# Kernel optimization log

Measured on AMD Instinct MI355X. Metric: run time of the kernel, lower is better.

Reference implementation:

```python
import jax, jax.numpy as jnp
from jax import lax
import numpy as np

UNTIL_T = 25  # until_time in source
EPS = 1e-6
K_SEG = 5     # number of temporal groups produced by Segment()


def conv1d(x, w, b=None, padding=((0, 0),)):
    y = lax.conv_general_dilated(x, w, (1,), padding,
                                 dimension_numbers=('NCH', 'OIH', 'NCH'))
    return y if b is None else y + b[None, :, None]


def maxpool1d(x, k, s):
    return lax.reduce_window(x, -jnp.inf, lax.max, (1, 1, k), (1, 1, s), 'VALID')


def batchnorm(x, g, b):
    m = x.mean((0, 2), keepdims=True)
    v = x.var((0, 2), keepdims=True)
    return g[None, :, None] * (x - m) / jnp.sqrt(v + 1e-5) + b[None, :, None]


def miu(x, sign, a, b):
    # fuzzy membership predicate: sigmoid(sign * a_c * (x - b_c))
    return jax.nn.sigmoid(sign * a[None, :, None] * (x - b[None, :, None]))


def upsample2(x):
    B, C, L = x.shape
    return jax.image.resize(x, (B, C, 2 * L), method='linear')


def logic_and(x, w, padding=((0, 0),)):
    # weighted geometric-mean fuzzy AND: exp(conv(log x, softmax(w)))
    wn = jax.nn.softmax(w.reshape(w.shape[0], -1), -1).reshape(w.shape)
    return jax.nn.relu(jnp.exp(conv1d(jnp.log(jnp.clip(x, 0.0, 1.0) + EPS), wn, padding=padding)))


def logic_or(x, w, padding=((0, 0),)):
    # dual fuzzy OR: 1 - exp(conv(log(1-x), softmax(w)))
    wn = jax.nn.softmax(w.reshape(w.shape[0], -1), -1).reshape(w.shape)
    return jax.nn.relu(1.0 - jnp.exp(conv1d(jnp.log(1.0 - jnp.clip(x, 0.0, 1.0) + EPS), wn, padding=padding)))


def until(x, T):
    # Until(x)[t] = max_{1<=d<=T} min( min_{0<=s<d} x[t+s], x[t+d] ), zero right-pad
    L = x.shape[-1]
    xp = jnp.pad(x, ((0, 0), (0, 0), (0, T)))
    runmin = x
    out = jnp.zeros_like(x)  # x >= 0 so 0 is a valid lower bound
    for d in range(1, T + 1):  # small fixed unroll over until_time
        xs = xp[..., d:d + L]
        out = jnp.maximum(out, jnp.minimum(runmin, xs))
        runmin = jnp.minimum(runmin, xs)
    return out[..., :L - 1]  # crop to match kernel-2 logic convs


def forward(x, wave_w, bn_g, bn_b, miu_ap, miu_bp, miu_an, miu_bn,
            ae_w1, ae_b1, ae_w2, ae_b2, ae_w3, ae_b3, ae_w4, ae_b4,
            and2_w, or2_w, and_w, or_w,
            fc1_w, fc1_b, fc2_w, fc2_b, fc3_w, fc3_b):
    B = x.shape[0]
    # Basic predicate network: wavelet conv (k=32) + BN + ReLU + pool -> [B,16,343]
    xf = maxpool1d(jax.nn.relu(batchnorm(conv1d(x, wave_w), bn_g, bn_b)), 3, 2)
    x_pos = maxpool1d(miu(xf, 1.0, miu_ap, miu_bp), 3, 2)    # [B,16,171]
    x_neg = maxpool1d(miu(xf, -1.0, miu_an, miu_bn), 3, 2)   # [B,16,171]
    x_miu = jnp.concatenate([x_pos, x_neg], 1)               # [B,32,171]
    # AutoEncoder -> w, same shape as x_miu
    h = maxpool1d(jnp.tanh(conv1d(x_miu, ae_w1, ae_b1, ((1, 1),))), 3, 2)   # [B,64,85]
    h = maxpool1d(jax.nn.relu(conv1d(h, ae_w2, ae_b2, ((1, 1),))), 3, 2)    # [B,32,42]
    h = jnp.tanh(conv1d(upsample2(h), ae_w3, ae_b3, ((2, 2),)))             # [B,64,86]
    h = jax.nn.sigmoid(conv1d(upsample2(h), ae_w4, ae_b4, ((2, 2),)))       # [B,32,174]
    w = maxpool1d(h, 4, 1)                                                  # [B,32,171]
    # Temporal grouping: K_SEG activation-level bands over w (vectorized, no cat loop)
    lo = (jnp.arange(K_SEG, dtype=w.dtype) / K_SEG)[:, None, None, None]
    hi = (jnp.arange(1, K_SEG + 1, dtype=w.dtype) / K_SEG).at[-1].set(2.0)[:, None, None, None]
    masks = (w[None] >= lo) & (w[None] < hi)                 # [K,B,32,171]
    seg = jnp.where(masks, w[None], 0.0) * x_miu[None]       # select_w * x_miu per segment
    inp = jnp.transpose(seg, (1, 0, 2, 3)).reshape(B, K_SEG * 32, -1)  # [B,160,171]
    x_until = until(inp, UNTIL_T)                            # [B,160,170]
    x_and1 = logic_and(inp, and2_w)                          # [B,20,170]
    x_or1 = logic_or(inp, or2_w)                             # [B,20,170]
    x1 = jnp.concatenate([x_and1, x_or1, x_until], 1)        # [B,200,170]
    x_and2 = logic_and(x1, and_w, ((1, 0),))                 # causal same-pad -> [B,6,170]
    x_or2 = logic_or(x1, or_w, ((1, 0),))                    # [B,6,170]
    x2 = jnp.concatenate([x_and2, x_or2], 1)                 # [B,12,170]
    # Classifier (dropout = identity at inference), Linear over last dim (=170)
    h = jax.nn.relu(jnp.einsum('bcl,ol->bco', x2, fc1_w) + fc1_b)
    h = jax.nn.relu(jnp.einsum('bco,po->bcp', h, fc2_w) + fc2_b)
    return jnp.einsum('bcp,qp->bcq', h, fc3_w) + fc3_b       # [B,12,10]


def setup_inputs() -> dict:
    key = jax.random.key(0)
    ks = jax.random.split(key, 24)
    n = lambda k, shp, s: jax.random.normal(k, shp, jnp.float32) * s
    B = 128
    d = {
        'x': n(ks[0], (B, 1, 719), 1.0),
        'wave_w': n(ks[1], (16, 1, 32), 1.0 / np.sqrt(32)),
        'bn_g': jnp.ones((16,), jnp.float32),
        'bn_b': jnp.zeros((16,), jnp.float32),
        'miu_ap': 1.0 + n(ks[2], (16,), 0.1),
        'miu_bp': n(ks[3], (16,), 0.1),
        'miu_an': 1.0 + n(ks[4], (16,), 0.1),
        'miu_bn': n(ks[5], (16,), 0.1),
        'ae_w1': n(ks[6], (64, 32, 3), 1.0 / np.sqrt(96)),
        'ae_b1': jnp.zeros((64,), jnp.float32),
        'ae_w2': n(ks[7], (32, 64, 3), 1.0 / np.sqrt(192)),
        'ae_b2': jnp.zeros((32,), jnp.float32),
        'ae_w3': n(ks[8], (64, 32, 3), 1.0 / np.sqrt(96)),
        'ae_b3': jnp.zeros((64,), jnp.float32),
        'ae_w4': n(ks[9], (32, 64, 3), 1.0 / np.sqrt(192)),
        'ae_b4': jnp.zeros((32,), jnp.float32),
        'and2_w': n(ks[10], (20, 160, 2), 1.0),
        'or2_w': n(ks[11], (20, 160, 2), 1.0),
        'and_w': n(ks[12], (6, 200, 2), 1.0),
        'or_w': n(ks[13], (6, 200, 2), 1.0),
        'fc1_w': n(ks[14], (1024, 170), 1.0 / np.sqrt(170)),
        'fc1_b': jnp.zeros((1024,), jnp.float32),
        'fc2_w': n(ks[15], (256, 1024), 1.0 / np.sqrt(1024)),
        'fc2_b': jnp.zeros((256,), jnp.float32),
        'fc3_w': n(ks[16], (10, 256), 1.0 / np.sqrt(256)),
        'fc3_b': jnp.zeros((10,), jnp.float32),
    }
    return d


def reference(x, wave_w, bn_g, bn_b, miu_ap, miu_bp, miu_an, miu_bn,
              ae_w1, ae_b1, ae_w2, ae_b2, ae_w3, ae_b3, ae_w4, ae_b4,
              and2_w, or2_w, and_w, or_w,
              fc1_w, fc1_b, fc2_w, fc2_b, fc3_w, fc3_b):
    return forward(x, wave_w, bn_g, bn_b, miu_ap, miu_bp, miu_an, miu_bn,
                   ae_w1, ae_b1, ae_w2, ae_b2, ae_w3, ae_b3, ae_w4, ae_b4,
                   and2_w, or2_w, and_w, or_w,
                   fc1_w, fc1_b, fc2_w, fc2_b, fc3_w, fc3_b)
```

## Files before the change

kernel.cpp:

```cpp
#include <hip/hip_runtime.h>

#define TPB 256
static inline int cdiv(int a, int b){ return (a + b - 1) / b; }

#define EPSL 1e-6f
#define ACT_TANH 0
#define ACT_RELU 1
#define ACT_SIG  2
#define ACT_NONE 3

__device__ __forceinline__ float sigf(float x){ return 1.0f / (1.0f + __expf(-x)); }
__device__ __forceinline__ float clip01(float x){ return fminf(fmaxf(x, 0.f), 1.f); }

#define OFF_Y1   0
#define OFF_XF   1409024
#define OFF_XMIU 2111488
#define OFF_H1   2811904
#define OFF_INP  4384768
#define OFF_X1   7886848
#define OFF_TAIL 12238848
#define OFF_P1   0
#define OFF_P2   0
#define OFF_GP   0
#define OFF_X2P  OFF_INP
#define OFF_W1P  (OFF_INP + 294912 + 393216)
#define OFF_FC1H OFF_X1
#define OFF_STATS OFF_TAIL
#define OFF_BNP  (OFF_TAIL + 64)
#define OFF_WN   (OFF_TAIL + 64 + 512)

__global__ void k_softmax(const float* __restrict__ a2, const float* __restrict__ o2,
                          const float* __restrict__ aw, const float* __restrict__ ow,
                          float* __restrict__ wn){
  int blk = blockIdx.x;
  const float* src; float* dst; int n;
  if (blk < 20)      { src = a2 + blk*320;      dst = wn + blk*320;              n = 320; }
  else if (blk < 40) { src = o2 + (blk-20)*320; dst = wn + 6400 + (blk-20)*320;  n = 320; }
  else if (blk < 46) { src = aw + (blk-40)*400; dst = wn + 12800 + (blk-40)*400; n = 400; }
  else               { src = ow + (blk-46)*400; dst = wn + 15200 + (blk-46)*400; n = 400; }
  __shared__ float sh[TPB];
  float m = -1e30f;
  for (int i = threadIdx.x; i < n; i += TPB) m = fmaxf(m, src[i]);
  sh[threadIdx.x] = m; __syncthreads();
  for (int off = TPB/2; off > 0; off >>= 1){
    if (threadIdx.x < off) sh[threadIdx.x] = fmaxf(sh[threadIdx.x], sh[threadIdx.x+off]);
    __syncthreads();
  }
  m = sh[0]; __syncthreads();
  float s = 0.f;
  for (int i = threadIdx.x; i < n; i += TPB) s += expf(src[i] - m);
  sh[threadIdx.x] = s; __syncthreads();
  for (int off = TPB/2; off > 0; off >>= 1){
    if (threadIdx.x < off) sh[threadIdx.x] += sh[threadIdx.x+off];
    __syncthreads();
  }
  float inv = 1.0f / sh[0];
  __syncthreads();
  for (int i = threadIdx.x; i < n; i += TPB) dst[i] = expf(src[i] - m) * inv;
}

__global__ void k_conv_wave(const float* __restrict__ x, const float* __restrict__ ww,
                            float* __restrict__ y){
  int idx = blockIdx.x*blockDim.x + threadIdx.x;
  if (idx >= 128*16*688) return;
  int l = idx % 688; int t = idx / 688; int o = t & 15; int b = t >> 4;
  const float* xr = x + b*719 + l;
  const float* wr = ww + o*32;
  float s = 0.f;
  #pragma unroll
  for (int k = 0; k < 32; k++) s = fmaf(xr[k], wr[k], s);
  y[idx] = s;
}

__global__ void k_bn_part(const float* __restrict__ y, double* __restrict__ bnp){
  int c = blockIdx.x & 15, ch = blockIdx.x >> 4;
  double s = 0.0, s2 = 0.0;
  for (int i = threadIdx.x; i < 16*688; i += TPB){
    int b = ch*16 + i/688, l = i % 688;
    float v = y[(b*16 + c)*688 + l];
    s += (double)v; s2 += (double)v * (double)v;
  }
  __shared__ double sh[TPB], sh2[TPB];
  sh[threadIdx.x] = s; sh2[threadIdx.x] = s2; __syncthreads();
  for (int off = TPB/2; off > 0; off >>= 1){
    if (threadIdx.x < off){ sh[threadIdx.x] += sh[threadIdx.x+off]; sh2[threadIdx.x] += sh2[threadIdx.x+off]; }
    __syncthreads();
  }
  if (threadIdx.x == 0){ bnp[blockIdx.x] = sh[0]; bnp[128 + blockIdx.x] = sh2[0]; }
}

__global__ void k_bn_fin(const double* __restrict__ bnp, float* __restrict__ stats){
  int c = threadIdx.x;
  if (c >= 16) return;
  double s = 0.0, s2 = 0.0;
  for (int j = 0; j < 8; j++){ s += bnp[j*16 + c]; s2 += bnp[128 + j*16 + c]; }
  double n = 128.0*688.0;
  double m = s / n;
  double var = s2 / n - m*m;
  stats[c]      = (float)m;
  stats[16 + c] = (float)(1.0 / sqrt(var + 1e-5));
}

__global__ void k_xmiu2(const float* __restrict__ y, const float* __restrict__ stats,
                        const float* __restrict__ g, const float* __restrict__ bb,
                        const float* __restrict__ ap, const float* __restrict__ bp,
                        const float* __restrict__ an, const float* __restrict__ bn,
                        float* __restrict__ out){
  int idx = blockIdx.x*blockDim.x + threadIdx.x;
  if (idx >= 128*32*171) return;
  int l = idx % 171; int t = idx / 171; int c = t & 31; int b = t >> 5;
  int cc = c & 15;
  float mean = stats[cc], rstd = stats[16 + cc];
  float gc = g[cc], bc = bb[cc];
  float sign = (c < 16) ? 1.f : -1.f;
  float a  = (c < 16) ? ap[cc] : an[cc];
  float bo = (c < 16) ? bp[cc] : bn[cc];
  const float* yr = y + (b*16 + cc)*688 + 4*l;
  float v[7];
  #pragma unroll
  for (int i = 0; i < 7; i++)
    v[i] = fmaxf(fmaf(gc*(yr[i] - mean), rstd, bc), 0.f);
  float m = -1e30f;
  #pragma unroll
  for (int j = 0; j < 3; j++){
    float xf = fmaxf(fmaxf(v[2*j], v[2*j+1]), v[2*j+2]);
    m = fmaxf(m, sigf(sign * a * (xf - bo)));
  }
  out[idx] = m;
}

template<int SMODE, int LSRC, int LEFF>
__device__ __forceinline__ float stage_val(const float* __restrict__ src, int q){
  if (q < 0 || q >= LEFF) return 0.f;
  if constexpr (SMODE == 0){
    return src[q];
  } else if constexpr (SMODE == 1){
    float m = fmaxf(fmaxf(src[2*q], src[2*q+1]), src[2*q+2]);
    return tanhf(m);
  } else if constexpr (SMODE == 2){
    auto P = [&](int k){
      float m = fmaxf(fmaxf(src[2*k], src[2*k+1]), src[2*k+2]);
      return fmaxf(m, 0.f);
    };
    if (q == 0) return P(0);
    if (q == LEFF - 1) return P(LEFF/2 - 1);
    int k = q >> 1;
    return (q & 1) ? 0.75f*P(k) + 0.25f*P(k+1) : 0.25f*P(k-1) + 0.75f*P(k);
  } else {
    if (q == 0) return src[0];
    if (q == LEFF - 1) return src[LSRC - 1];
    int k = q >> 1;
    return (q & 1) ? 0.75f*src[k] + 0.25f*src[k+1] : 0.25f*src[k-1] + 0.75f*src[k];
  }
}

template<int CIN, int LSRC, int LEFF, int COUT, int LOUT, int PAD, int ACT, int PL, int SMODE>
__global__ void __launch_bounds__(256) k_conv(const float* __restrict__ in,
                                              const float* __restrict__ w,
                                              const float* __restrict__ bias,
                                              float* __restrict__ outp){
  constexpr int LSEG = 4*PL;
  constexpr int WL = ((LSEG + 2) + 3) & ~3;
  constexpr int K3 = CIN*3;
  __shared__ float smem[CIN*WL + 8 + K3*COUT];
  float* sin = smem;
  float* wT  = smem + CIN*WL + 8;
  const int b = blockIdx.x;
  const int tid = threadIdx.x;
  const int base = blockIdx.y*LSEG - PAD;

  const float* gin = in + b*CIN*LSRC;
  for (int e = tid; e < CIN*WL; e += 256){
    int i = e / WL, c = e - i*WL;
    sin[e] = stage_val<SMODE, LSRC, LEFF>(gin + i*LSRC, base + c);
  }
  if (tid < 8) sin[CIN*WL + tid] = 0.f;
  for (int e = tid; e < K3*COUT; e += 256){
    int o = e & (COUT-1), m = e / COUT;
    wT[m*COUT + o] = w[o*K3 + m];
  }
  __syncthreads();

  const int to = tid / PL, tp = tid - (tid/PL)*PL;
  const int o0 = to*4;
  const int pl0 = 4*tp;
  float acc[4][4] = {{0,0,0,0},{0,0,0,0},{0,0,0,0},{0,0,0,0}};

  for (int i = 0; i < CIN; i++){
    const float* srow = sin + i*WL + pl0;
    float xv[6];
    *(float4*)&xv[0] = *(const float4*)srow;
    *(float2*)&xv[4] = *(const float2*)(srow + 4);
    const float* wrow = wT + (i*3)*COUT + o0;
    float wv[3][4];
    #pragma unroll
    for (int k = 0; k < 3; k++)
      *(float4*)&wv[k][0] = *(const float4*)(wrow + k*COUT);
    #pragma unroll
    for (int j = 0; j < 4; j++)
      #pragma unroll
      for (int k = 0; k < 3; k++)
        #pragma unroll
        for (int oo = 0; oo < 4; oo++)
          acc[j][oo] = fmaf(xv[j+k], wv[k][oo], acc[j][oo]);
  }

  const int pg0 = blockIdx.y*LSEG + pl0;
  float bv[4];
  #pragma unroll
  for (int oo = 0; oo < 4; oo++) bv[oo] = bias[o0 + oo];
  #pragma unroll
  for (int oo = 0; oo < 4; oo++){
    float* orow = outp + (b*COUT + o0 + oo)*LOUT;
    #pragma unroll
    for (int j = 0; j < 4; j++){
      int p = pg0 + j;
      if (p < LOUT){
        float s = acc[j][oo] + bv[oo];
        float r;
        if (ACT == ACT_TANH)      r = tanhf(s);
        else if (ACT == ACT_RELU) r = fmaxf(s, 0.f);
        else if (ACT == ACT_SIG)  r = sigf(s);
        else                      r = s;
        orow[p] = r;
      }
    }
  }
}

__global__ void k_inp(const float* __restrict__ h4, const float* __restrict__ xmiu,
                      float* __restrict__ inp){
  int idx = blockIdx.x*blockDim.x + threadIdx.x;
  if (idx >= 128*32*171) return;
  int l = idx % 171; int t = idx / 171; int c = t & 31; int b = t >> 5;
  const float* hr = h4 + t*174 + l;
  float wv = fmaxf(fmaxf(hr[0], hr[1]), fmaxf(hr[2], hr[3]));
  float xm = xmiu[idx];
  float prod = wv * xm;
  const float lo[5] = {0.0f, 0.2f, 0.4f, 0.6f, 0.8f};
  const float hi[5] = {0.2f, 0.4f, 0.6f, 0.8f, 2.0f};
  float* op = inp + ((b*160) + c)*171 + l;
  #pragma unroll
  for (int s = 0; s < 5; s++){
    bool m = (wv >= lo[s]) && (wv < hi[s]);
    op[s*32*171] = m ? prod : 0.f;
  }
}

__global__ void k_until(const float* __restrict__ inp, float* __restrict__ x1){
  int idx = blockIdx.x*blockDim.x + threadIdx.x;
  if (idx >= 128*160*170) return;
  int l = idx % 170; int t = idx / 170; int c = t % 160; int b = t / 160;
  const float* xr = inp + (b*160 + c)*171;
  float runmin = xr[l];
  float outv = 0.f;
  #pragma unroll 5
  for (int d = 1; d <= 25; d++){
    float xs = (l + d < 171) ? xr[l + d] : 0.f;
    outv = fmaxf(outv, fminf(runmin, xs));
    runmin = fminf(runmin, xs);
  }
  x1[((b*200) + 40 + c)*170 + l] = outv;
}

__global__ void __launch_bounds__(TPB) k_logic1p(const float* __restrict__ inp, const float* __restrict__ wn,
                                                 float* __restrict__ p1){
  int bl = blockIdx.x*TPB + threadIdx.x;
  int l = bl % 170; int b = bl / 170;
  int ch = blockIdx.y, v = blockIdx.z;
  const float* W = wn + (v ? 6400 : 0);
  float acc[20];
  #pragma unroll
  for (int o = 0; o < 20; o++) acc[o] = 0.f;
  int c0 = ch*40;
  const float* ir = inp + (b*160 + c0)*171 + l;
  for (int c = 0; c < 40; c++){
    float u0 = clip01(ir[0]);
    float u1 = clip01(ir[1]);
    float g0, g1;
    if (v){ g0 = __logf(1.f - u0 + EPSL); g1 = __logf(1.f - u1 + EPSL); }
    else  { g0 = __logf(u0 + EPSL);       g1 = __logf(u1 + EPSL); }
    const float* wc = W + 2*(c0 + c);
    #pragma unroll
    for (int o = 0; o < 20; o++)
      acc[o] = fmaf(wc[o*320], g0, fmaf(wc[o*320 + 1], g1, acc[o]));
    ir += 171;
  }
  float* pp = p1 + ((ch*128 + b)*40 + v*20)*170 + l;
  #pragma unroll
  for (int o = 0; o < 20; o++) pp[o*170] = acc[o];
}

__global__ void k_fin1(const float* __restrict__ p1, float* __restrict__ x1){
  int idx = blockIdx.x*blockDim.x + threadIdx.x;
  if (idx >= 128*40*170) return;
  int l = idx % 170; int o = (idx/170) % 40; int b = idx / (170*40);
  float s = 0.f;
  #pragma unroll
  for (int ch = 0; ch < 4; ch++) s += p1[((ch*128 + b)*40 + o)*170 + l];
  float e = __expf(s);
  float r = (o < 20) ? e : fmaxf(0.f, 1.f - e);
  x1[(b*200 + o)*170 + l] = r;
}

__global__ void __launch_bounds__(TPB) k_logic2p(const float* __restrict__ x1, const float* __restrict__ wn,
                                                 float* __restrict__ p2){
  int bl = blockIdx.x*TPB + threadIdx.x;
  int l = bl % 170; int b = bl / 170;
  int ch = blockIdx.y, v = blockIdx.z;
  const float* W = wn + 12800 + (v ? 2400 : 0);
  float acc[6] = {0.f,0.f,0.f,0.f,0.f,0.f};
  int c0 = ch*50;
  const float* xr = x1 + (b*200 + c0)*170 + l;
  for (int c = 0; c < 50; c++){
    float g0 = 0.f;
    if (l > 0){
      float u0 = clip01(xr[-1]);
      g0 = v ? __logf(1.f - u0 + EPSL) : __logf(u0 + EPSL);
    }
    float u1 = clip01(xr[0]);
    float g1 = v ? __logf(1.f - u1 + EPSL) : __logf(u1 + EPSL);
    const float* wc = W + 2*(c0 + c);
    #pragma unroll
    for (int o = 0; o < 6; o++)
      acc[o] = fmaf(wc[o*400], g0, fmaf(wc[o*400 + 1], g1, acc[o]));
    xr += 170;
  }
  float* pp = p2 + ((ch*128 + b)*12 + v*6)*170 + l;
  #pragma unroll
  for (int o = 0; o < 6; o++) pp[o*170] = acc[o];
}

__global__ void k_prep(const float* __restrict__ p2, const float* __restrict__ w,
                       float* __restrict__ x2p, float* __restrict__ wp){
  int idx = blockIdx.x*blockDim.x + threadIdx.x;
  if (idx < 1024*192){
    int k = idx % 192; int o = idx / 192;
    wp[idx] = (k < 170) ? w[o*170 + k] : 0.f;
    return;
  }
  idx -= 1024*192;
  if (idx >= 128*12*192) return;
  int l = idx % 192; int ro = idx / 192;
  if (l >= 170){ x2p[ro*192 + l] = 0.f; return; }
  int o = ro % 12; int b = ro / 12;
  float s = 0.f;
  #pragma unroll
  for (int ch = 0; ch < 4; ch++) s += p2[((ch*128 + b)*12 + o)*170 + l];
  float e = __expf(s);
  float r = (o < 6) ? e : fmaxf(0.f, 1.f - e);
  x2p[ro*192 + l] = r;
}

template<int M, int N, int K, int KSPLIT>
__global__ void __launch_bounds__(256) k_gemm(const float* __restrict__ A,
                                              const float* __restrict__ W,
                                              float* __restrict__ C){
  static_assert(K % (KSPLIT*32) == 0, "K split");
  constexpr int KC = K / KSPLIT;
  constexpr int NT = KC / 32;
  constexpr int S = 68;
  __shared__ float As[2][32*S];
  __shared__ float Bs[2][32*S];
  const int m0 = blockIdx.x*64, n0 = blockIdx.y*64;
  const int kbeg = blockIdx.z*KC;
  const int tid = threadIdx.x;
  const int row = tid >> 2;
  const int c4  = (tid & 3)*4;
  const int tm  = (tid & 15)*4;
  const int tn  = (tid >> 4)*4;

  const float* Ar = A + (m0 + row)*K + kbeg + c4;
  const float* Wr = W + (n0 + row)*K + kbeg + c4;

  float4 ra0 = *(const float4*)(Ar);
  float4 ra1 = *(const float4*)(Ar + 16);
  float4 rb0 = *(const float4*)(Wr);
  float4 rb1 = *(const float4*)(Wr + 16);

  float acc[4][4] = {{0,0,0,0},{0,0,0,0},{0,0,0,0},{0,0,0,0}};
  int buf = 0;
  {
    float* a = As[0]; float* b = Bs[0];
    #pragma unroll
    for (int i = 0; i < 4; i++){
      a[(c4 + i)*S + row]      = ((const float*)&ra0)[i];
      a[(c4 + 16 + i)*S + row] = ((const float*)&ra1)[i];
      b[(c4 + i)*S + row]      = ((const float*)&rb0)[i];
      b[(c4 + 16 + i)*S + row] = ((const float*)&rb1)[i];
    }
  }
  __syncthreads();

  for (int t = 0; t < NT; t++){
    if (t + 1 < NT){
      Ar += 32; Wr += 32;
      ra0 = *(const float4*)(Ar);
      ra1 = *(const float4*)(Ar + 16);
      rb0 = *(const float4*)(Wr);
      rb1 = *(const float4*)(Wr + 16);
    }
    const float* a = As[buf]; const float* b = Bs[buf];
    #pragma unroll
    for (int k = 0; k < 32; k++){
      const float4 av = *(const float4*)(a + k*S + tm);
      const float4 bv = *(const float4*)(b + k*S + tn);
      acc[0][0] = fmaf(av.x, bv.x, acc[0][0]); acc[0][1] = fmaf(av.x, bv.y, acc[0][1]);
      acc[0][2] = fmaf(av.x, bv.z, acc[0][2]); acc[0][3] = fmaf(av.x, bv.w, acc[0][3]);
      acc[1][0] = fmaf(av.y, bv.x, acc[1][0]); acc[1][1] = fmaf(av.y, bv.y, acc[1][1]);
      acc[1][2] = fmaf(av.y, bv.z, acc[1][2]); acc[1][3] = fmaf(av.y, bv.w, acc[1][3]);
      acc[2][0] = fmaf(av.z, bv.x, acc[2][0]); acc[2][1] = fmaf(av.z, bv.y, acc[2][1]);
      acc[2][2] = fmaf(av.z, bv.z, acc[2][2]); acc[2][3] = fmaf(av.z, bv.w, acc[2][3]);
      acc[3][0] = fmaf(av.w, bv.x, acc[3][0]); acc[3][1] = fmaf(av.w, bv.y, acc[3][1]);
      acc[3][2] = fmaf(av.w, bv.z, acc[3][2]); acc[3][3] = fmaf(av.w, bv.w, acc[3][3]);
    }
    if (t + 1 < NT){
      int nb = buf ^ 1;
      float* an = As[nb]; float* bn = Bs[nb];
      #pragma unroll
      for (int i = 0; i < 4; i++){
        an[(c4 + i)*S + row]      = ((const float*)&ra0)[i];
        an[(c4 + 16 + i)*S + row] = ((const float*)&ra1)[i];
        bn[(c4 + i)*S + row]      = ((const float*)&rb0)[i];
        bn[(c4 + 16 + i)*S + row] = ((const float*)&rb1)[i];
      }
      __syncthreads();
      buf = nb;
    }
  }

  float* Cz = C + (size_t)blockIdx.z*M*N;
  #pragma unroll
  for (int i = 0; i < 4; i++){
    float4 v = {acc[i][0], acc[i][1], acc[i][2], acc[i][3]};
    *(float4*)&Cz[(m0 + tm + i)*N + n0 + tn] = v;
  }
}

template<int MN, int N, int KS>
__global__ void k_comb(const float* __restrict__ part, const float* __restrict__ bias,
                       float* __restrict__ out){
  int idx = blockIdx.x*blockDim.x + threadIdx.x;
  if (idx >= MN) return;
  int n = idx % N;
  float s = bias[n];
  #pragma unroll
  for (int z = 0; z < KS; z++) s += part[(size_t)z*MN + idx];
  out[idx] = fmaxf(s, 0.f);
}

__global__ void __launch_bounds__(256) k_tail(const float* __restrict__ gp,
                                              const float* __restrict__ b2,
                                              const float* __restrict__ w3,
                                              const float* __restrict__ b3,
                                              float* __restrict__ out){
  constexpr int MN = 1536*256;
  __shared__ float sh[256];
  __shared__ float ps[160];
  const int row = blockIdx.x;
  const int t = threadIdx.x;
  float s = b2[t];
  #pragma unroll
  for (int z = 0; z < 8; z++) s += gp[(size_t)z*MN + row*256 + t];
  sh[t] = fmaxf(s, 0.f);
  __syncthreads();
  if (t < 160){
    int q = t >> 4, j = t & 15;
    const float* wr = w3 + q*256 + j*16;
    const float* hr = sh + j*16;
    float p = 0.f;
    #pragma unroll
    for (int i = 0; i < 16; i++) p = fmaf(hr[i], wr[i], p);
    ps[t] = p;
  }
  __syncthreads();
  if (t < 10){
    float s3 = b3[t];
    #pragma unroll
    for (int j = 0; j < 16; j++) s3 += ps[t*16 + j];
    out[row*10 + t] = s3;
  }
}

extern "C" void kernel_launch(void* const* d_in, const int* in_sizes, int n_in,
                              void* d_out, int out_size, void* d_ws, size_t ws_size,
                              hipStream_t stream) {
  const float* x      = (const float*)d_in[0];
  const float* wave_w = (const float*)d_in[1];
  const float* bn_g   = (const float*)d_in[2];
  const float* bn_b   = (const float*)d_in[3];
  const float* miu_ap = (const float*)d_in[4];
  const float* miu_bp = (const float*)d_in[5];
  const float* miu_an = (const float*)d_in[6];
  const float* miu_bn = (const float*)d_in[7];
  const float* ae_w1  = (const float*)d_in[8];
  const float* ae_b1  = (const float*)d_in[9];
  const float* ae_w2  = (const float*)d_in[10];
  const float* ae_b2  = (const float*)d_in[11];
  const float* ae_w3  = (const float*)d_in[12];
  const float* ae_b3  = (const float*)d_in[13];
  const float* ae_w4  = (const float*)d_in[14];
  const float* ae_b4  = (const float*)d_in[15];
  const float* and2_w = (const float*)d_in[16];
  const float* or2_w  = (const float*)d_in[17];
  const float* and_w  = (const float*)d_in[18];
  const float* or_w   = (const float*)d_in[19];
  const float* fc1_w  = (const float*)d_in[20];
  const float* fc1_b  = (const float*)d_in[21];
  const float* fc2_w  = (const float*)d_in[22];
  const float* fc2_b  = (const float*)d_in[23];
  const float* fc3_w  = (const float*)d_in[24];
  const float* fc3_b  = (const float*)d_in[25];
  float* out = (float*)d_out;
  float* ws  = (float*)d_ws;

  float* y1    = ws + OFF_Y1;
  float* xmiu  = ws + OFF_XMIU;
  float* c1    = ws + OFF_H1;
  float* c2    = ws + OFF_XF;
  float* h3    = ws + OFF_Y1;
  float* h4    = ws + OFF_H1;
  float* inp   = ws + OFF_INP;
  float* x1    = ws + OFF_X1;
  float* p1    = ws + OFF_P1;
  float* p2    = ws + OFF_P2;
  float* gp    = ws + OFF_GP;
  float* x2p   = ws + OFF_X2P;
  float* w1p   = ws + OFF_W1P;
  float* fc1h  = ws + OFF_FC1H;
  float* stats = ws + OFF_STATS;
  double* bnp  = (double*)(ws + OFF_BNP);
  float* wn    = ws + OFF_WN;

  k_softmax  <<<52, TPB, 0, stream>>>(and2_w, or2_w, and_w, or_w, wn);
  k_conv_wave<<<cdiv(128*16*688, TPB), TPB, 0, stream>>>(x, wave_w, y1);
  k_bn_part  <<<128, TPB, 0, stream>>>(y1, bnp);
  k_bn_fin   <<<1, 64, 0, stream>>>(bnp, stats);
  k_xmiu2    <<<cdiv(128*32*171, TPB), TPB, 0, stream>>>(y1, stats, bn_g, bn_b,
                                                         miu_ap, miu_bp, miu_an, miu_bn, xmiu);

  k_conv<32,171,171,64,171,1,ACT_NONE,16,0><<<dim3(128,3), 256, 0, stream>>>(xmiu, ae_w1, ae_b1, c1);
  k_conv<64,171, 85,32, 85,1,ACT_NONE,32,1><<<dim3(128,1), 256, 0, stream>>>(c1, ae_w2, ae_b2, c2);
  k_conv<32, 85, 84,64, 86,2,ACT_TANH,16,2><<<dim3(128,2), 256, 0, stream>>>(c2, ae_w3, ae_b3, h3);
  k_conv<64, 86,172,32,174,2,ACT_SIG ,32,3><<<dim3(128,2), 256, 0, stream>>>(h3, ae_w4, ae_b4, h4);

  k_inp      <<<cdiv(128*32*171, TPB), TPB, 0, stream>>>(h4, xmiu, inp);
  k_until    <<<cdiv(128*160*170,TPB), TPB, 0, stream>>>(inp, x1);
  k_logic1p  <<<dim3(85, 4, 2), TPB, 0, stream>>>(inp, wn, p1);
  k_fin1     <<<cdiv(128*40*170, TPB), TPB, 0, stream>>>(p1, x1);
  k_logic2p  <<<dim3(85, 4, 2), TPB, 0, stream>>>(x1, wn, p2);
  k_prep     <<<cdiv(1024*192 + 128*12*192, TPB), TPB, 0, stream>>>(p2, fc1_w, x2p, w1p);

  k_gemm<1536,1024,192,2><<<dim3(24,16,2), 256, 0, stream>>>(x2p, w1p, gp);
  k_comb<1536*1024,1024,2><<<cdiv(1536*1024, TPB), TPB, 0, stream>>>(gp, fc1_b, fc1h);
  k_gemm<1536,256,1024,8><<<dim3(24,4,8), 256, 0, stream>>>(fc1h, fc2_w, gp);
  k_tail     <<<1536, 256, 0, stream>>>(gp, fc2_b, fc3_w, fc3_b, out);
}
```

Measured before the change: 358.7 us.

## Merge small kernels and fold epilogues to cut launch count

Combines softmax, wavelet conv and fc1 weight padding into one multi-role launch. The BN finalisation moves into k_xmiu2, until runs in the same launch as logic1 partials, and the fin1 reduction is folded into logic2 so it reads p1 directly. fc1's GEMM drops its K split and applies bias+ReLU in its epilogue, removing k_comb, and fc2's split goes from 8 to 4. The aim is less launch overhead and fewer partial-sum round trips through memory, at the cost of fewer blocks per GEMM and redundant exp/reduction work in logic2.

```diff
diff --git a/kernel.cpp b/kernel.cpp
--- a/kernel.cpp
+++ b/kernel.cpp
@@ -20,56 +20,61 @@
 #define OFF_X1   7886848
 #define OFF_TAIL 12238848
 #define OFF_P1   0
-#define OFF_P2   0
+#define OFF_P2   (OFF_INP + 400000)
 #define OFF_GP   0
 #define OFF_X2P  OFF_INP
-#define OFF_W1P  (OFF_INP + 294912 + 393216)
 #define OFF_FC1H OFF_X1
 #define OFF_STATS OFF_TAIL
 #define OFF_BNP  (OFF_TAIL + 64)
 #define OFF_WN   (OFF_TAIL + 64 + 512)
-
-__global__ void k_softmax(const float* __restrict__ a2, const float* __restrict__ o2,
-                          const float* __restrict__ aw, const float* __restrict__ ow,
-                          float* __restrict__ wn){
-  int blk = blockIdx.x;
-  const float* src; float* dst; int n;
-  if (blk < 20)      { src = a2 + blk*320;      dst = wn + blk*320;              n = 320; }
-  else if (blk < 40) { src = o2 + (blk-20)*320; dst = wn + 6400 + (blk-20)*320;  n = 320; }
-  else if (blk < 46) { src = aw + (blk-40)*400; dst = wn + 12800 + (blk-40)*400; n = 400; }
-  else               { src = ow + (blk-46)*400; dst = wn + 15200 + (blk-46)*400; n = 400; }
-  __shared__ float sh[TPB];
-  float m = -1e30f;
-  for (int i = threadIdx.x; i < n; i += TPB) m = fmaxf(m, src[i]);
-  sh[threadIdx.x] = m; __syncthreads();
-  for (int off = TPB/2; off > 0; off >>= 1){
-    if (threadIdx.x < off) sh[threadIdx.x] = fmaxf(sh[threadIdx.x], sh[threadIdx.x+off]);
+#define OFF_W1P  (OFF_TAIL + 64 + 512 + 17600)
+
+__global__ void __launch_bounds__(TPB) k_misc(const float* __restrict__ a2, const float* __restrict__ o2,
+                     const float* __restrict__ aw, const float* __restrict__ ow,
+                     float* __restrict__ wn,
+                     const float* __restrict__ x, const float* __restrict__ ww,
+                     float* __restrict__ y,
+                     const float* __restrict__ w1, float* __restrict__ wp){
+  int bid = blockIdx.x;
+  if (bid < 52){
+    const float* src; float* dst; int n;
+    if (bid < 20)      { src = a2 + bid*320;      dst = wn + bid*320;              n = 320; }
+    else if (bid < 40) { src = o2 + (bid-20)*320; dst = wn + 6400 + (bid-20)*320;  n = 320; }
+    else if (bid < 46) { src = aw + (bid-40)*400; dst = wn + 12800 + (bid-40)*400; n = 400; }
+    else               { src = ow + (bid-46)*400; dst = wn + 15200 + (bid-46)*400; n = 400; }
+    __shared__ float sh[TPB];
+    float m = -1e30f;
+    for (int i = threadIdx.x; i < n; i += TPB) m = fmaxf(m, src[i]);
+    sh[threadIdx.x] = m; __syncthreads();
+    for (int off = TPB/2; off > 0; off >>= 1){
+      if (threadIdx.x < off) sh[threadIdx.x] = fmaxf(sh[threadIdx.x], sh[threadIdx.x+off]);
+      __syncthreads();
+    }
+    m = sh[0]; __syncthreads();
+    float s = 0.f;
+    for (int i = threadIdx.x; i < n; i += TPB) s += expf(src[i] - m);
+    sh[threadIdx.x] = s; __syncthreads();
+    for (int off = TPB/2; off > 0; off >>= 1){
+      if (threadIdx.x < off) sh[threadIdx.x] += sh[threadIdx.x+off];
+      __syncthreads();
+    }
+    float inv = 1.0f / sh[0];
     __syncthreads();
-  }
-  m = sh[0]; __syncthreads();
-  float s = 0.f;
-  for (int i = threadIdx.x; i < n; i += TPB) s += expf(src[i] - m);
-  sh[threadIdx.x] = s; __syncthreads();
-  for (int off = TPB/2; off > 0; off >>= 1){
-    if (threadIdx.x < off) sh[threadIdx.x] += sh[threadIdx.x+off];
-    __syncthreads();
-  }
-  float inv = 1.0f / sh[0];
-  __syncthreads();
-  for (int i = threadIdx.x; i < n; i += TPB) dst[i] = expf(src[i] - m) * inv;
-}
-
-__global__ void k_conv_wave(const float* __restrict__ x, const float* __restrict__ ww,
-                            float* __restrict__ y){
-  int idx = blockIdx.x*blockDim.x + threadIdx.x;
-  if (idx >= 128*16*688) return;
-  int l = idx % 688; int t = idx / 688; int o = t & 15; int b = t >> 4;
-  const float* xr = x + b*719 + l;
-  const float* wr = ww + o*32;
-  float s = 0.f;
-  #pragma unroll
-  for (int k = 0; k < 32; k++) s = fmaf(xr[k], wr[k], s);
-  y[idx] = s;
+    for (int i = threadIdx.x; i < n; i += TPB) dst[i] = expf(src[i] - m) * inv;
+  } else if (bid < 52 + 5504){
+    int idx = (bid - 52)*TPB + threadIdx.x;
+    int l = idx % 688; int t = idx / 688; int o = t & 15; int b = t >> 4;
+    const float* xr = x + b*719 + l;
+    const float* wr = ww + o*32;
+    float s = 0.f;
+    #pragma unroll
+    for (int k = 0; k < 32; k++) s = fmaf(xr[k], wr[k], s);
+    y[idx] = s;
+  } else {
+    int idx = (bid - 5556)*TPB + threadIdx.x;
+    int k = idx % 192; int o = idx / 192;
+    wp[idx] = (k < 170) ? w1[o*170 + k] : 0.f;
+  }
 }
 
 __global__ void k_bn_part(const float* __restrict__ y, double* __restrict__ bnp){
@@ -89,28 +94,29 @@
   if (threadIdx.x == 0){ bnp[blockIdx.x] = sh[0]; bnp[128 + blockIdx.x] = sh2[0]; }
 }
 
-__global__ void k_bn_fin(const double* __restrict__ bnp, float* __restrict__ stats){
-  int c = threadIdx.x;
-  if (c >= 16) return;
-  double s = 0.0, s2 = 0.0;
-  for (int j = 0; j < 8; j++){ s += bnp[j*16 + c]; s2 += bnp[128 + j*16 + c]; }
-  double n = 128.0*688.0;
-  double m = s / n;
-  double var = s2 / n - m*m;
-  stats[c]      = (float)m;
-  stats[16 + c] = (float)(1.0 / sqrt(var + 1e-5));
-}
-
-__global__ void k_xmiu2(const float* __restrict__ y, const float* __restrict__ stats,
+__global__ void k_xmiu2(const float* __restrict__ y, const double* __restrict__ bnp,
                         const float* __restrict__ g, const float* __restrict__ bb,
                         const float* __restrict__ ap, const float* __restrict__ bp,
                         const float* __restrict__ an, const float* __restrict__ bn,
                         float* __restrict__ out){
+  __shared__ float smean[16], srstd[16];
+  if (threadIdx.x < 16){
+    int cc = threadIdx.x;
+    double s = 0.0, s2 = 0.0;
+    #pragma unroll
+    for (int j = 0; j < 8; j++){ s += bnp[j*16 + cc]; s2 += bnp[128 + j*16 + cc]; }
+    double n = 128.0*688.0;
+    double m = s / n;
+    double var = s2 / n - m*m;
+    smean[cc] = (float)m;
+    srstd[cc] = (float)(1.0 / sqrt(var + 1e-5));
+  }
+  __syncthreads();
   int idx = blockIdx.x*blockDim.x + threadIdx.x;
   if (idx >= 128*32*171) return;
   int l = idx % 171; int t = idx / 171; int c = t & 31; int b = t >> 5;
   int cc = c & 15;
-  float mean = stats[cc], rstd = stats[16 + cc];
+  float mean = smean[cc], rstd = srstd[cc];
   float gc = g[cc], bc = bb[cc];
   float sign = (c < 16) ? 1.f : -1.f;
   float a  = (c < 16) ? ap[cc] : an[cc];
@@ -247,99 +253,99 @@
   }
 }
 
-__global__ void k_until(const float* __restrict__ inp, float* __restrict__ x1){
-  int idx = blockIdx.x*blockDim.x + threadIdx.x;
-  if (idx >= 128*160*170) return;
-  int l = idx % 170; int t = idx / 170; int c = t % 160; int b = t / 160;
-  const float* xr = inp + (b*160 + c)*171;
-  float runmin = xr[l];
-  float outv = 0.f;
-  #pragma unroll 5
-  for (int d = 1; d <= 25; d++){
-    float xs = (l + d < 171) ? xr[l + d] : 0.f;
-    outv = fmaxf(outv, fminf(runmin, xs));
-    runmin = fminf(runmin, xs);
-  }
-  x1[((b*200) + 40 + c)*170 + l] = outv;
-}
-
-__global__ void __launch_bounds__(TPB) k_logic1p(const float* __restrict__ inp, const float* __restrict__ wn,
-                                                 float* __restrict__ p1){
-  int bl = blockIdx.x*TPB + threadIdx.x;
-  int l = bl % 170; int b = bl / 170;
-  int ch = blockIdx.y, v = blockIdx.z;
-  const float* W = wn + (v ? 6400 : 0);
-  float acc[20];
-  #pragma unroll
-  for (int o = 0; o < 20; o++) acc[o] = 0.f;
-  int c0 = ch*40;
-  const float* ir = inp + (b*160 + c0)*171 + l;
-  for (int c = 0; c < 40; c++){
-    float u0 = clip01(ir[0]);
-    float u1 = clip01(ir[1]);
-    float g0, g1;
-    if (v){ g0 = __logf(1.f - u0 + EPSL); g1 = __logf(1.f - u1 + EPSL); }
-    else  { g0 = __logf(u0 + EPSL);       g1 = __logf(u1 + EPSL); }
-    const float* wc = W + 2*(c0 + c);
-    #pragma unroll
-    for (int o = 0; o < 20; o++)
-      acc[o] = fmaf(wc[o*320], g0, fmaf(wc[o*320 + 1], g1, acc[o]));
-    ir += 171;
-  }
-  float* pp = p1 + ((ch*128 + b)*40 + v*20)*170 + l;
-  #pragma unroll
-  for (int o = 0; o < 20; o++) pp[o*170] = acc[o];
-}
-
-__global__ void k_fin1(const float* __restrict__ p1, float* __restrict__ x1){
-  int idx = blockIdx.x*blockDim.x + threadIdx.x;
-  if (idx >= 128*40*170) return;
-  int l = idx % 170; int o = (idx/170) % 40; int b = idx / (170*40);
-  float s = 0.f;
-  #pragma unroll
-  for (int ch = 0; ch < 4; ch++) s += p1[((ch*128 + b)*40 + o)*170 + l];
-  float e = __expf(s);
-  float r = (o < 20) ? e : fmaxf(0.f, 1.f - e);
-  x1[(b*200 + o)*170 + l] = r;
-}
-
-__global__ void __launch_bounds__(TPB) k_logic2p(const float* __restrict__ x1, const float* __restrict__ wn,
-                                                 float* __restrict__ p2){
+__global__ void __launch_bounds__(TPB) k_ul1(const float* __restrict__ inp, const float* __restrict__ wn,
+                                             float* __restrict__ x1, float* __restrict__ p1){
+  int bid = blockIdx.x;
+  if (bid < 13600){
+    int idx = bid*TPB + threadIdx.x;
+    int l = idx % 170; int t = idx / 170; int c = t % 160; int b = t / 160;
+    const float* xr = inp + (b*160 + c)*171;
+    float runmin = xr[l];
+    float outv = 0.f;
+    #pragma unroll 5
+    for (int d = 1; d <= 25; d++){
+      float xs = (l + d < 171) ? xr[l + d] : 0.f;
+      outv = fmaxf(outv, fminf(runmin, xs));
+      runmin = fminf(runmin, xs);
+    }
+    x1[((b*200) + 40 + c)*170 + l] = outv;
+  } else {
+    int r = bid - 13600;
+    int xb = r % 85; int rr = r / 85; int ch = rr & 3; int v = rr >> 2;
+    int bl = xb*TPB + threadIdx.x;
+    int l = bl % 170; int b = bl / 170;
+    const float* W = wn + (v ? 6400 : 0);
+    float acc[20];
+    #pragma unroll
+    for (int o = 0; o < 20; o++) acc[o] = 0.f;
+    int c0 = ch*40;
+    const float* ir = inp + (b*160 + c0)*171 + l;
+    for (int c = 0; c < 40; c++){
+      float u0 = clip01(ir[0]);
+      float u1 = clip01(ir[1]);
+      float g0, g1;
+      if (v){ g0 = __logf(1.f - u0 + EPSL); g1 = __logf(1.f - u1 + EPSL); }
+      else  { g0 = __logf(u0 + EPSL);       g1 = __logf(u1 + EPSL); }
+      const float* wc = W + 2*(c0 + c);
+      #pragma unroll
+      for (int o = 0; o < 20; o++)
+        acc[o] = fmaf(wc[o*320], g0, fmaf(wc[o*320 + 1], g1, acc[o]));
+      ir += 171;
+    }
+    float* pp = p1 + ((ch*128 + b)*40 + v*20)*170 + l;
+    #pragma unroll
+    for (int o = 0; o < 20; o++) pp[o*170] = acc[o];
+  }
+}
+
+__global__ void __launch_bounds__(TPB) k_logic2p(const float* __restrict__ x1, const float* __restrict__ p1,
+                                                 const float* __restrict__ wn, float* __restrict__ p2){
   int bl = blockIdx.x*TPB + threadIdx.x;
   int l = bl % 170; int b = bl / 170;
   int ch = blockIdx.y, v = blockIdx.z;
   const float* W = wn + 12800 + (v ? 2400 : 0);
   float acc[6] = {0.f,0.f,0.f,0.f,0.f,0.f};
   int c0 = ch*50;
-  const float* xr = x1 + (b*200 + c0)*170 + l;
-  for (int c = 0; c < 50; c++){
+  bool have0 = (l > 0);
+  for (int c = c0; c < c0 + 50; c++){
+    float u0 = 0.f, u1;
+    if (c < 40){
+      float s1 = 0.f;
+      #pragma unroll
+      for (int q = 0; q < 4; q++) s1 += p1[((q*128 + b)*40 + c)*170 + l];
+      float e = __expf(s1);
+      u1 = (c < 20) ? e : fmaxf(0.f, 1.f - e);
+      if (have0){
+        float s0 = 0.f;
+        #pragma unroll
+        for (int q = 0; q < 4; q++) s0 += p1[((q*128 + b)*40 + c)*170 + l - 1];
+        float e0 = __expf(s0);
+        u0 = (c < 20) ? e0 : fmaxf(0.f, 1.f - e0);
+      }
+    } else {
+      const float* xr = x1 + (b*200 + c)*170 + l;
+      u1 = xr[0];
+      if (have0) u0 = xr[-1];
+    }
     float g0 = 0.f;
-    if (l > 0){
-      float u0 = clip01(xr[-1]);
-      g0 = v ? __logf(1.f - u0 + EPSL) : __logf(u0 + EPSL);
-    }
-    float u1 = clip01(xr[0]);
-    float g1 = v ? __logf(1.f - u1 + EPSL) : __logf(u1 + EPSL);
-    const float* wc = W + 2*(c0 + c);
+    if (have0){
+      float uc = clip01(u0);
+      g0 = v ? __logf(1.f - uc + EPSL) : __logf(uc + EPSL);
+    }
+    float uc1 = clip01(u1);
+    float g1 = v ? __logf(1.f - uc1 + EPSL) : __logf(uc1 + EPSL);
+    const float* wc = W + 2*c;
     #pragma unroll
     for (int o = 0; o < 6; o++)
       acc[o] = fmaf(wc[o*400], g0, fmaf(wc[o*400 + 1], g1, acc[o]));
-    xr += 170;
   }
   float* pp = p2 + ((ch*128 + b)*12 + v*6)*170 + l;
   #pragma unroll
   for (int o = 0; o < 6; o++) pp[o*170] = acc[o];
 }
 
-__global__ void k_prep(const float* __restrict__ p2, const float* __restrict__ w,
-                       float* __restrict__ x2p, float* __restrict__ wp){
+__global__ void k_fin2(const float* __restrict__ p2, float* __restrict__ x2p){
   int idx = blockIdx.x*blockDim.x + threadIdx.x;
-  if (idx < 1024*192){
-    int k = idx % 192; int o = idx / 192;
-    wp[idx] = (k < 170) ? w[o*170 + k] : 0.f;
-    return;
-  }
-  idx -= 1024*192;
   if (idx >= 128*12*192) return;
   int l = idx % 192; int ro = idx / 192;
   if (l >= 170){ x2p[ro*192 + l] = 0.f; return; }
@@ -352,9 +358,10 @@
   x2p[ro*192 + l] = r;
 }
 
-template<int M, int N, int K, int KSPLIT>
+template<int M, int N, int K, int KSPLIT, int ACT>
 __global__ void __launch_bounds__(256) k_gemm(const float* __restrict__ A,
                                               const float* __restrict__ W,
+                                              const float* __restrict__ bias,
                                               float* __restrict__ C){
   static_assert(K % (KSPLIT*32) == 0, "K split");
   constexpr int KC = K / KSPLIT;
@@ -429,24 +436,28 @@
     }
   }
 
-  float* Cz = C + (size_t)blockIdx.z*M*N;
-  #pragma unroll
-  for (int i = 0; i < 4; i++){
-    float4 v = {acc[i][0], acc[i][1], acc[i][2], acc[i][3]};
-    *(float4*)&Cz[(m0 + tm + i)*N + n0 + tn] = v;
-  }
-}
-
-template<int MN, int N, int KS>
-__global__ void k_comb(const float* __restrict__ part, const float* __restrict__ bias,
-                       float* __restrict__ out){
-  int idx = blockIdx.x*blockDim.x + threadIdx.x;
-  if (idx >= MN) return;
-  int n = idx % N;
-  float s = bias[n];
-  #pragma unroll
-  for (int z = 0; z < KS; z++) s += part[(size_t)z*MN + idx];
-  out[idx] = fmaxf(s, 0.f);
+  if (KSPLIT == 1){
+    #pragma unroll
+    for (int i = 0; i < 4; i++){
+      float4 vv;
+      vv.x = acc[i][0] + bias[n0 + tn];
+      vv.y = acc[i][1] + bias[n0 + tn + 1];
+      vv.z = acc[i][2] + bias[n0 + tn + 2];
+      vv.w = acc[i][3] + bias[n0 + tn + 3];
+      if (ACT == ACT_RELU){
+        vv.x = fmaxf(vv.x, 0.f); vv.y = fmaxf(vv.y, 0.f);
+        vv.z = fmaxf(vv.z, 0.f); vv.w = fmaxf(vv.w, 0.f);
+      }
+      *(float4*)&C[(m0 + tm + i)*N + n0 + tn] = vv;
+    }
+  } else {
+    float* Cz = C + (size_t)blockIdx.z*M*N;
+    #pragma unroll
+    for (int i = 0; i < 4; i++){
+      float4 vv = {acc[i][0], acc[i][1], acc[i][2], acc[i][3]};
+      *(float4*)&Cz[(m0 + tm + i)*N + n0 + tn] = vv;
+    }
+  }
 }
 
 __global__ void __launch_bounds__(256) k_tail(const float* __restrict__ gp,
@@ -461,7 +472,7 @@
   const int t = threadIdx.x;
   float s = b2[t];
   #pragma unroll
-  for (int z = 0; z < 8; z++) s += gp[(size_t)z*MN + row*256 + t];
+  for (int z = 0; z < 4; z++) s += gp[(size_t)z*MN + row*256 + t];
   sh[t] = fmaxf(s, 0.f);
   __syncthreads();
   if (t < 160){
@@ -528,15 +539,13 @@
   float* x2p   = ws + OFF_X2P;
   float* w1p   = ws + OFF_W1P;
   float* fc1h  = ws + OFF_FC1H;
-  float* stats = ws + OFF_STATS;
   double* bnp  = (double*)(ws + OFF_BNP);
   float* wn    = ws + OFF_WN;
 
-  k_softmax  <<<52, TPB, 0, stream>>>(and2_w, or2_w, and_w, or_w, wn);
-  k_conv_wave<<<cdiv(128*16*688, TPB), TPB, 0, stream>>>(x, wave_w, y1);
+  k_misc     <<<52 + 5504 + 768, TPB, 0, stream>>>(and2_w, or2_w, and_w, or_w, wn,
+                                                   x, wave_w, y1, fc1_w, w1p);
   k_bn_part  <<<128, TPB, 0, stream>>>(y1, bnp);
-  k_bn_fin   <<<1, 64, 0, stream>>>(bnp, stats);
-  k_xmiu2    <<<cdiv(128*32*171, TPB), TPB, 0, stream>>>(y1, stats, bn_g, bn_b,
+  k_xmiu2    <<<cdiv(128*32*171, TPB), TPB, 0, stream>>>(y1, bnp, bn_g, bn_b,
                                                          miu_ap, miu_bp, miu_an, miu_bn, xmiu);
 
   k_conv<32,171,171,64,171,1,ACT_NONE,16,0><<<dim3(128,3), 256, 0, stream>>>(xmiu, ae_w1, ae_b1, c1);
@@ -545,14 +554,11 @@
   k_conv<64, 86,172,32,174,2,ACT_SIG ,32,3><<<dim3(128,2), 256, 0, stream>>>(h3, ae_w4, ae_b4, h4);
 
   k_inp      <<<cdiv(128*32*171, TPB), TPB, 0, stream>>>(h4, xmiu, inp);
-  k_until    <<<cdiv(128*160*170,TPB), TPB, 0, stream>>>(inp, x1);
-  k_logic1p  <<<dim3(85, 4, 2), TPB, 0, stream>>>(inp, wn, p1);
-  k_fin1     <<<cdiv(128*40*170, TPB), TPB, 0, stream>>>(p1, x1);
-  k_logic2p  <<<dim3(85, 4, 2), TPB, 0, stream>>>(x1, wn, p2);
-  k_prep     <<<cdiv(1024*192 + 128*12*192, TPB), TPB, 0, stream>>>(p2, fc1_w, x2p, w1p);
-
-  k_gemm<1536,1024,192,2><<<dim3(24,16,2), 256, 0, stream>>>(x2p, w1p, gp);
-  k_comb<1536*1024,1024,2><<<cdiv(1536*1024, TPB), TPB, 0, stream>>>(gp, fc1_b, fc1h);
-  k_gemm<1536,256,1024,8><<<dim3(24,4,8), 256, 0, stream>>>(fc1h, fc2_w, gp);
+  k_ul1      <<<13600 + 680, TPB, 0, stream>>>(inp, wn, x1, p1);
+  k_logic2p  <<<dim3(85, 4, 2), TPB, 0, stream>>>(x1, p1, wn, p2);
+  k_fin2     <<<cdiv(128*12*192, TPB), TPB, 0, stream>>>(p2, x2p);
+
+  k_gemm<1536,1024,192,1,ACT_RELU><<<dim3(24,16,1), 256, 0, stream>>>(x2p, w1p, fc1_b, fc1h);
+  k_gemm<1536,256,1024,4,ACT_NONE><<<dim3(24,4,4), 256, 0, stream>>>(fc1h, fc2_w, fc2_b, gp);
   k_tail     <<<1536, 256, 0, stream>>>(gp, fc2_b, fc3_w, fc3_b, out);
 }
```

New measurement: 345.0 us. 1.04x faster.
